# Performance work log

Hardware: AMD Instinct MI355X
Metric: run time of the kernel (lower is better)

The kernel has to match this reference:

```python
import jax, jax.numpy as jnp
import numpy as np

S, N, CM, CZ, H, D = 512, 768, 64, 128, 8, 32
EPS = 1e-5


def _layer_norm(x, w, b):
    mu = jnp.mean(x, axis=-1, keepdims=True)
    xc = x - mu
    var = jnp.mean(xc * xc, axis=-1, keepdims=True)
    return xc * jax.lax.rsqrt(var + EPS) * w + b


def setup_inputs() -> dict:
    key = jax.random.key(0)
    ks = jax.random.split(key, 6)
    scale_m = 1.0 / np.sqrt(CM)
    scale_z = 1.0 / np.sqrt(CZ)
    scale_o = 1.0 / np.sqrt(H * D)
    return {
        "m": jax.random.normal(ks[0], (1, S, N, CM), jnp.float32),
        "z": jax.random.normal(ks[1], (1, N, N, CZ), jnp.float32),
        "norm_m_w": jnp.ones((CM,), jnp.float32),
        "norm_m_b": jnp.zeros((CM,), jnp.float32),
        "norm_z_w": jnp.ones((CZ,), jnp.float32),
        "norm_z_b": jnp.zeros((CZ,), jnp.float32),
        "wm": jax.random.normal(ks[2], (CM, H * D), jnp.float32) * scale_m,
        "wg": jax.random.normal(ks[3], (CM, H * D), jnp.float32) * scale_m,
        "wz": jax.random.normal(ks[4], (CZ, H), jnp.float32) * scale_z,
        "wo": jax.random.normal(ks[5], (H * D, CM), jnp.float32) * scale_o,
    }


def reference(m, z, norm_m_w, norm_m_b, norm_z_w, norm_z_b, wm, wg, wz, wo):
    m0 = m[0]  # [S, N, CM]
    z0 = z[0]  # [N, N, CZ]
    mn = _layer_norm(m0, norm_m_w, norm_m_b)
    zn = _layer_norm(z0, norm_z_w, norm_z_b)
    # b[p,q,h]; original code softmaxes over the LAST axis of b'[h,p,q] (axis q)
    # but contracts as o[s,q] = sum_p w[p,q] v[s,p] (transpose_a matmul),
    # so softmax is over axis q = axis 1 of [p,q,h].
    b = jnp.einsum('pqc,ch->pqh', zn, wz)
    w = jax.nn.softmax(b, axis=1)  # normalized over q for each p (faithful to source)
    v = jnp.einsum('spc,ck->spk', mn, wm).reshape(S, N, H, D)
    g = jax.nn.sigmoid(jnp.einsum('spc,ck->spk', mn, wg)).reshape(S, N, H, D)
    o = jnp.einsum('pqh,sphd->sqhd', w, v) * g  # weighted average then gate
    out = jnp.einsum('sqhd,hdc->sqc', o, wo.reshape(H, D, CM))
    return out[None]  # [1, S, N, CM]
```

## Files before the change

### kernel.cpp

```cpp
#include <hip/hip_runtime.h>
#include <hip/hip_bf16.h>
#include <stdint.h>

#define S_DIM 512
#define N_DIM 768
#define CMd   64
#define CZd   128
#define Hd    8
#define Dd    32
#define HDd   256

typedef float          f32x4  __attribute__((ext_vector_type(4)));
typedef __bf16         bf16x8 __attribute__((ext_vector_type(8)));
typedef unsigned int   u32x4  __attribute__((ext_vector_type(4)));
typedef unsigned int   u32x2  __attribute__((ext_vector_type(2)));
typedef unsigned short u16x8  __attribute__((ext_vector_type(8)));

__device__ __forceinline__ unsigned short f2bf(float f) {
  __bf16 h = (__bf16)f;
  return __builtin_bit_cast(unsigned short, h);
}
__device__ __forceinline__ float bf2f(unsigned short u) {
  unsigned int x = ((unsigned int)u) << 16;
  return __builtin_bit_cast(float, x);
}
__device__ __forceinline__ float sigmoidf_(float x) {
  return 1.f / (1.f + __expf(-x));
}

__global__ __launch_bounds__(256) void k0_prep(const float* __restrict__ wm,
                                               const float* __restrict__ wg,
                                               const float* __restrict__ wo,
                                               unsigned short* __restrict__ WBT,
                                               unsigned short* __restrict__ woT) {
  int t = blockIdx.x * 256 + threadIdx.x;
  if (t < 512 * 64) {
    int j = t >> 6, c = t & 63;
    float v = (j < 256) ? wm[c * 256 + j] : wg[c * 256 + (j - 256)];
    WBT[t] = f2bf(v);
  }
  if (t < 64 * 256) {
    int c = t >> 8, k = t & 255;
    woT[t] = f2bf(wo[k * 64 + c]);
  }
}

__global__ __launch_bounds__(256) void k1_zln_b(const float* __restrict__ z,
                                                const float* __restrict__ nzw,
                                                const float* __restrict__ nzb,
                                                const float* __restrict__ wz,
                                                float* __restrict__ b_e) {
  __shared__ float wzT[8][128];
  int t = threadIdx.x;
  for (int i = t; i < 1024; i += 256) {
    int h = i >> 7, c = i & 127;
    wzT[h][c] = wz[c * 8 + h];
  }
  __syncthreads();

  int lane = t & 63, w = t >> 6;
  int sub = lane & 7;
  int rloc = lane >> 3;
  int p = blockIdx.y;
  int q = blockIdx.x * 32 + w * 8 + rloc;

  const float* zr = z + ((size_t)p * N_DIM + q) * CZd + sub * 16;
  f32x4 v[4];
#pragma unroll
  for (int j = 0; j < 4; j++) v[j] = *(const f32x4*)(zr + 4 * j);

  float s1 = 0.f, s2 = 0.f;
#pragma unroll
  for (int j = 0; j < 4; j++)
#pragma unroll
    for (int e = 0; e < 4; e++) { float x = v[j][e]; s1 += x; s2 += x * x; }
  s1 += __shfl_xor(s1, 1); s2 += __shfl_xor(s2, 1);
  s1 += __shfl_xor(s1, 2); s2 += __shfl_xor(s2, 2);
  s1 += __shfl_xor(s1, 4); s2 += __shfl_xor(s2, 4);
  float mean = s1 * (1.f / 128.f);
  float var  = s2 * (1.f / 128.f) - mean * mean;
  float rstd = rsqrtf(var + 1e-5f);

  const float* wp = nzw + sub * 16;
  const float* bp = nzb + sub * 16;
  float zn[16];
#pragma unroll
  for (int j = 0; j < 4; j++) {
    f32x4 wv = *(const f32x4*)(wp + 4 * j);
    f32x4 bv = *(const f32x4*)(bp + 4 * j);
#pragma unroll
    for (int e = 0; e < 4; e++)
      zn[j * 4 + e] = (v[j][e] - mean) * rstd * wv[e] + bv[e];
  }

  float accb[8];
#pragma unroll
  for (int h = 0; h < 8; h++) {
    const f32x4* wr = (const f32x4*)&wzT[h][sub * 16];
    float a = 0.f;
#pragma unroll
    for (int j = 0; j < 4; j++) {
      f32x4 ww = wr[j];
#pragma unroll
      for (int e = 0; e < 4; e++) a += zn[j * 4 + e] * ww[e];
    }
    accb[h] = a;
  }
#pragma unroll
  for (int mask = 1; mask <= 4; mask <<= 1)
#pragma unroll
    for (int h = 0; h < 8; h++) accb[h] += __shfl_xor(accb[h], mask);

  float outv = accb[0];
#pragma unroll
  for (int h = 1; h < 8; h++) outv = (sub == h) ? accb[h] : outv;
  b_e[((size_t)p * 8 + sub) * 768 + q] = outv;
}

__global__ __launch_bounds__(256) void k1b_softmax(float* __restrict__ b_e,
                                                   float* __restrict__ invs) {
  int row = blockIdx.x;
  int t = threadIdx.x;
  float* base = b_e + (size_t)row * 768;
  float x0 = base[t], x1 = base[t + 256], x2 = base[t + 512];
  __shared__ float red[256];
  red[t] = fmaxf(x0, fmaxf(x1, x2));
  __syncthreads();
  for (int o = 128; o > 0; o >>= 1) {
    if (t < o) red[t] = fmaxf(red[t], red[t + o]);
    __syncthreads();
  }
  float M = red[0];
  __syncthreads();
  float e0 = __expf(x0 - M), e1 = __expf(x1 - M), e2 = __expf(x2 - M);
  base[t] = e0; base[t + 256] = e1; base[t + 512] = e2;
  red[t] = e0 + e1 + e2;
  __syncthreads();
  for (int o = 128; o > 0; o >>= 1) {
    if (t < o) red[t] += red[t + o];
    __syncthreads();
  }
  if (t == 0) invs[row] = 1.0f / red[0];
}

__global__ __launch_bounds__(256) void k1b2_transpose(const float* __restrict__ b_e,
                                                      const float* __restrict__ invs,
                                                      unsigned short* __restrict__ Aw) {
  int t = threadIdx.x;
  int q0 = blockIdx.x * 64, p0 = blockIdx.y * 64, h = blockIdx.z;
  __shared__ unsigned short T[64][65];
  int i = t >> 2, ch = t & 3;
  size_t rowid = (size_t)(p0 + i) * 8 + h;
  const float* src = b_e + rowid * 768 + q0 + ch * 16;
  float inv = invs[rowid];
#pragma unroll
  for (int jj = 0; jj < 16; jj += 4) {
    f32x4 v = *(const f32x4*)(src + jj);
#pragma unroll
    for (int e = 0; e < 4; e++) T[i][ch * 16 + jj + e] = f2bf(v[e] * inv);
  }
  __syncthreads();
  int j = i;
  unsigned short outv[16];
#pragma unroll
  for (int ii = 0; ii < 16; ii++) outv[ii] = T[ch * 16 + ii][j];
  unsigned short* dst = Aw + ((size_t)h * 768 + q0 + j) * 768 + p0 + ch * 16;
  *(u32x4*)(dst)     = *(u32x4*)(outv);
  *(u32x4*)(dst + 8) = *(u32x4*)(outv + 8);
}

__global__ __launch_bounds__(256) void k2_mln_vg(const float* __restrict__ mp,
                                                 const float* __restrict__ nmw,
                                                 const float* __restrict__ nmb,
                                                 const unsigned short* __restrict__ WBT,
                                                 unsigned short* __restrict__ VT,
                                                 unsigned short* __restrict__ G) {
  __shared__ unsigned short WBs[512 * 64];
  __shared__ unsigned short As[64 * 64];
  int t = threadIdx.x;
  int p0 = blockIdx.x * 64, s = blockIdx.y;

#pragma unroll
  for (int it = 0; it < 16; it++) {
    int cid = t + it * 256;
    int row = cid >> 3, ch = cid & 7;
    u32x4 v = *(const u32x4*)(WBT + row * 64 + ch * 8);
    *(u32x4*)(WBs + row * 64 + ((ch * 8) ^ ((row & 7) << 3))) = v;
  }

  {
    int row = t >> 2, qt = t & 3;
    const float* mr = mp + ((size_t)s * N_DIM + p0 + row) * CMd + qt * 16;
    f32x4 v[4];
#pragma unroll
    for (int j = 0; j < 4; j++) v[j] = *(const f32x4*)(mr + 4 * j);
    float s1 = 0.f, s2 = 0.f;
#pragma unroll
    for (int j = 0; j < 4; j++)
#pragma unroll
      for (int e = 0; e < 4; e++) { float x = v[j][e]; s1 += x; s2 += x * x; }
    s1 += __shfl_xor(s1, 1); s2 += __shfl_xor(s2, 1);
    s1 += __shfl_xor(s1, 2); s2 += __shfl_xor(s2, 2);
    float mean = s1 * (1.f / 64.f);
    float var  = s2 * (1.f / 64.f) - mean * mean;
    float rstd = rsqrtf(var + 1e-5f);
    unsigned short o[16];
#pragma unroll
    for (int j = 0; j < 4; j++) {
      f32x4 wv = *(const f32x4*)(nmw + qt * 16 + 4 * j);
      f32x4 bv = *(const f32x4*)(nmb + qt * 16 + 4 * j);
#pragma unroll
      for (int e = 0; e < 4; e++)
        o[j * 4 + e] = f2bf((v[j][e] - mean) * rstd * wv[e] + bv[e]);
    }
    int k0 = qt * 16;
    *(u32x4*)(As + row * 64 + ((k0) ^ ((row & 7) << 3)))     = *(u32x4*)(o);
    *(u32x4*)(As + row * 64 + ((k0 + 8) ^ ((row & 7) << 3))) = *(u32x4*)(o + 8);
  }
  __syncthreads();

  int lane = t & 63, w = t >> 6;
  int n0 = w * 128;
  int lr = lane & 15, lk8 = (lane >> 4) * 8;
  f32x4 zero = {0.f, 0.f, 0.f, 0.f};
  f32x4 acc[4][8];
#pragma unroll
  for (int i = 0; i < 4; i++)
#pragma unroll
    for (int j = 0; j < 8; j++) acc[i][j] = zero;

#pragma unroll
  for (int kk = 0; kk < 2; kk++) {
    bf16x8 bfr[8];
#pragma unroll
    for (int nt = 0; nt < 8; nt++) {
      int r = n0 + nt * 16 + lr;
      bfr[nt] = *(const bf16x8*)(WBs + r * 64 + ((kk * 32 + lk8) ^ ((r & 7) << 3)));
    }
#pragma unroll
    for (int mt = 0; mt < 4; mt++) {
      int ar = mt * 16 + lr;
      bf16x8 a = *(const bf16x8*)(As + ar * 64 + ((kk * 32 + lk8) ^ ((ar & 7) << 3)));
#pragma unroll
      for (int nt = 0; nt < 8; nt++)
        acc[mt][nt] = __builtin_amdgcn_mfma_f32_16x16x32_bf16(a, bfr[nt], acc[mt][nt], 0, 0, 0);
    }
  }

#pragma unroll
  for (int mt = 0; mt < 4; mt++)
#pragma unroll
    for (int nt = 0; nt < 8; nt++) {
      int j = n0 + nt * 16 + lr;
      int ploc = mt * 16 + (lane >> 4) * 4;
      if (j < 256) {
        int h = j >> 5, d = j & 31;
        unsigned short pk[4];
#pragma unroll
        for (int r = 0; r < 4; r++) pk[r] = f2bf(acc[mt][nt][r]);
        *(u32x2*)(VT + ((size_t)h * 16384 + s * 32 + d) * 768 + p0 + ploc) = *(u32x2*)pk;
      } else {
        int jj = j - 256;
#pragma unroll
        for (int r = 0; r < 4; r++)
          G[((size_t)s * 768 + p0 + ploc + r) * 256 + jj] = f2bf(sigmoidf_(acc[mt][nt][r]));
      }
    }
}

__global__ __launch_bounds__(256) void k3_gemm(const unsigned short* __restrict__ Aw,
                                               const unsigned short* __restrict__ VT,
                                               unsigned short* __restrict__ O) {
  __shared__ unsigned short Asl[128 * 64];
  __shared__ unsigned short Bsl[128 * 64];
  int t = threadIdx.x;
  int flat = blockIdx.x;
  int h = blockIdx.y;
  int f2 = (flat & 7) * 96 + (flat >> 3);
  int mt_b = f2 % 6, nt_b = f2 / 6;
  int q0 = mt_b * 128, n0 = nt_b * 128;

  const unsigned short* Ab = Aw + (size_t)h * 768 * 768 + (size_t)q0 * 768;
  const unsigned short* Bb = VT + (size_t)h * 16384 * 768 + (size_t)n0 * 768;

  int lane = t & 63, w = t >> 6;
  int wr = (w >> 1) * 64, wc = (w & 1) * 64;
  int lr = lane & 15, lk8 = (lane >> 4) * 8;
  int ch = t & 7, r0 = t >> 3;

  u32x4 ra[4], rb[4];
#pragma unroll
  for (int it = 0; it < 4; it++) {
    int r = r0 + it * 32;
    ra[it] = *(const u32x4*)(Ab + (size_t)r * 768 + ch * 8);
    rb[it] = *(const u32x4*)(Bb + (size_t)r * 768 + ch * 8);
  }

  f32x4 zero = {0.f, 0.f, 0.f, 0.f};
  f32x4 acc[4][4];
#pragma unroll
  for (int i = 0; i < 4; i++)
#pragma unroll
    for (int j = 0; j < 4; j++) acc[i][j] = zero;

  for (int kt = 0; kt < 12; kt++) {
#pragma unroll
    for (int it = 0; it < 4; it++) {
      int cid = t + it * 256;
      int row = cid >> 3, c = cid & 7;
      int idx = row * 64 + ((c * 8) ^ ((row & 7) << 3));
      *(u32x4*)(Asl + idx) = ra[it];
      *(u32x4*)(Bsl + idx) = rb[it];
    }
    __syncthreads();
    if (kt < 11) {
      int k0 = (kt + 1) * 64;
#pragma unroll
      for (int it = 0; it < 4; it++) {
        int r = r0 + it * 32;
        ra[it] = *(const u32x4*)(Ab + (size_t)r * 768 + k0 + ch * 8);
        rb[it] = *(const u32x4*)(Bb + (size_t)r * 768 + k0 + ch * 8);
      }
    }
#pragma unroll
    for (int kk = 0; kk < 2; kk++) {
      bf16x8 afr[4], bfr[4];
#pragma unroll
      for (int i = 0; i < 4; i++) {
        int arr = wr + i * 16 + lr;
        int brr = wc + i * 16 + lr;
        afr[i] = *(const bf16x8*)(Asl + arr * 64 + ((kk * 32 + lk8) ^ ((arr & 7) << 3)));
        bfr[i] = *(const bf16x8*)(Bsl + brr * 64 + ((kk * 32 + lk8) ^ ((brr & 7) << 3)));
      }
#pragma unroll
      for (int mt = 0; mt < 4; mt++)
#pragma unroll
        for (int nt = 0; nt < 4; nt++)
          acc[mt][nt] = __builtin_amdgcn_mfma_f32_16x16x32_bf16(afr[mt], bfr[nt], acc[mt][nt], 0, 0, 0);
    }
    __syncthreads();
  }

#pragma unroll
  for (int mt = 0; mt < 4; mt++)
#pragma unroll
    for (int nt = 0; nt < 4; nt++) {
      int q = q0 + wr + mt * 16 + (lane >> 4) * 4;
      int n = n0 + wc + nt * 16 + lr;
      int s_ = n >> 5, d = n & 31;
      size_t ob = ((size_t)s_ * 768 + q) * 256 + h * 32 + d;
#pragma unroll
      for (int r = 0; r < 4; r++)
        O[ob + (size_t)r * 256] = f2bf(acc[mt][nt][r]);
    }
}

__global__ __launch_bounds__(256) void k4_out(const unsigned short* __restrict__ O,
                                              const unsigned short* __restrict__ G,
                                              const unsigned short* __restrict__ woT,
                                              float* __restrict__ out) {
  __shared__ unsigned short OGs[64 * 256];
  __shared__ unsigned short WOs[64 * 256];
  int t = threadIdx.x;
  int q0 = blockIdx.x * 64, s = blockIdx.y;

#pragma unroll
  for (int it = 0; it < 8; it++) {
    int cid = t + it * 256;
    int row = cid >> 5, ch = cid & 31;
    u32x4 v = *(const u32x4*)(woT + row * 256 + ch * 8);
    *(u32x4*)(WOs + row * 256 + ((ch * 8) ^ ((row & 7) << 3))) = v;
  }

  int i = t >> 2, c4 = t & 3;
  const unsigned short* Orow = O + ((size_t)s * 768 + q0 + i) * 256 + c4 * 64;
  const unsigned short* Grow = G + ((size_t)s * 768 + q0 + i) * 256 + c4 * 64;
#pragma unroll
  for (int jj = 0; jj < 8; jj++) {
    u16x8 ov = *(const u16x8*)(Orow + jj * 8);
    u16x8 gv = *(const u16x8*)(Grow + jj * 8);
    unsigned short pk[8];
#pragma unroll
    for (int e = 0; e < 8; e++) pk[e] = f2bf(bf2f(ov[e]) * bf2f(gv[e]));
    *(u32x4*)(OGs + i * 256 + ((c4 * 64 + jj * 8) ^ ((i & 7) << 3))) = *(u32x4*)pk;
  }
  __syncthreads();

  int lane = t & 63, w = t >> 6;
  int lr = lane & 15, lk8 = (lane >> 4) * 8;
  f32x4 zero = {0.f, 0.f, 0.f, 0.f};
  f32x4 acc[4];
#pragma unroll
  for (int nt = 0; nt < 4; nt++) acc[nt] = zero;

#pragma unroll
  for (int kk = 0; kk < 8; kk++) {
    int ar = w * 16 + lr;
    bf16x8 a = *(const bf16x8*)(OGs + ar * 256 + ((kk * 32 + lk8) ^ ((ar & 7) << 3)));
#pragma unroll
    for (int nt = 0; nt < 4; nt++) {
      int br = nt * 16 + lr;
      bf16x8 b = *(const bf16x8*)(WOs + br * 256 + ((kk * 32 + lk8) ^ ((br & 7) << 3)));
      acc[nt] = __builtin_amdgcn_mfma_f32_16x16x32_bf16(a, b, acc[nt], 0, 0, 0);
    }
  }

#pragma unroll
  for (int nt = 0; nt < 4; nt++) {
    int q = q0 + w * 16 + (lane >> 4) * 4;
    int c = nt * 16 + lr;
    float* dst = out + ((size_t)s * 768 + q) * 64 + c;
#pragma unroll
    for (int r = 0; r < 4; r++) dst[(size_t)r * 64] = acc[nt][r];
  }
}

extern "C" void kernel_launch(void* const* d_in, const int* in_sizes, int n_in,
                              void* d_out, int out_size, void* d_ws, size_t ws_size,
                              hipStream_t stream) {
  const float* m   = (const float*)d_in[0];
  const float* z   = (const float*)d_in[1];
  const float* nmw = (const float*)d_in[2];
  const float* nmb = (const float*)d_in[3];
  const float* nzw = (const float*)d_in[4];
  const float* nzb = (const float*)d_in[5];
  const float* wm  = (const float*)d_in[6];
  const float* wg  = (const float*)d_in[7];
  const float* wz  = (const float*)d_in[8];
  const float* wo  = (const float*)d_in[9];
  float* out = (float*)d_out;

  char* ws = (char*)d_ws;
  size_t off = 0;
  auto alloc = [&](size_t bytes) -> void* {
    void* p = ws + off;
    off += (bytes + 1023) & ~(size_t)1023;
    return p;
  };
  float*          b_e  = (float*)alloc((size_t)768 * 8 * 768 * 4);
  float*          invs = (float*)alloc((size_t)768 * 8 * 4);
  unsigned short* Awt  = (unsigned short*)alloc((size_t)8 * 768 * 768 * 2);
  unsigned short* WBT  = (unsigned short*)alloc((size_t)512 * 64 * 2);
  unsigned short* woT  = (unsigned short*)alloc((size_t)64 * 256 * 2);
  unsigned short* VT   = (unsigned short*)alloc((size_t)8 * 16384 * 768 * 2);
  unsigned short* G    = (unsigned short*)alloc((size_t)512 * 768 * 256 * 2);
  unsigned short* O    = (unsigned short*)alloc((size_t)512 * 768 * 256 * 2);
  if (ws_size < off) return;

  k0_prep<<<128, 256, 0, stream>>>(wm, wg, wo, WBT, woT);
  k1_zln_b<<<dim3(24, 768), 256, 0, stream>>>(z, nzw, nzb, wz, b_e);
  k1b_softmax<<<6144, 256, 0, stream>>>(b_e, invs);
  k1b2_transpose<<<dim3(12, 12, 8), 256, 0, stream>>>(b_e, invs, Awt);
  k2_mln_vg<<<dim3(12, 512), 256, 0, stream>>>(m, nmw, nmb, WBT, VT, G);
  k3_gemm<<<dim3(768, 8), 256, 0, stream>>>(Awt, VT, O);
  k4_out<<<dim3(12, 512), 256, 0, stream>>>(O, G, woT, out);
}
```

Baseline: 693.5 us.

## Load GEMM tiles directly into LDS with global_load_lds using pre-swizzled layouts

The producer kernels now write Aw and VT in a layout that is already XOR-swizzled within each 64-element block. This lets the main GEMM copy tiles straight from global memory into LDS with 16-byte global_load_lds, with no register staging and no swizzle at LDS-write time. The aim is to save VGPRs and LDS write instructions. In exchange, the old register prefetch of the next k-tile is gone: each iteration waits on vmcnt(0) before computing, so load latency is no longer overlapped with MFMA work, and the layout is now coupled across kernels.

```diff
diff --git a/kernel.cpp b/kernel.cpp
--- a/kernel.cpp
+++ b/kernel.cpp
@@ -26,6 +26,12 @@
 }
 __device__ __forceinline__ float sigmoidf_(float x) {
   return 1.f / (1.f + __expf(-x));
+}
+
+typedef __attribute__((address_space(1))) const void cg_void;
+typedef __attribute__((address_space(3))) void lds_void;
+__device__ __forceinline__ void async16(const unsigned short* g, unsigned short* l) {
+  __builtin_amdgcn_global_load_lds((cg_void*)g, (lds_void*)l, 16, 0, 0);
 }
 
 __global__ __launch_bounds__(256) void k0_prep(const float* __restrict__ wm,
@@ -164,9 +170,10 @@
   unsigned short outv[16];
 #pragma unroll
   for (int ii = 0; ii < 16; ii++) outv[ii] = T[ch * 16 + ii][j];
-  unsigned short* dst = Aw + ((size_t)h * 768 + q0 + j) * 768 + p0 + ch * 16;
-  *(u32x4*)(dst)     = *(u32x4*)(outv);
-  *(u32x4*)(dst + 8) = *(u32x4*)(outv + 8);
+  int rx = (j & 7) << 3;
+  unsigned short* dstrow = Aw + ((size_t)h * 768 + q0 + j) * 768 + p0;
+  *(u32x4*)(dstrow + ((ch * 16) ^ rx))     = *(u32x4*)(outv);
+  *(u32x4*)(dstrow + ((ch * 16 + 8) ^ rx)) = *(u32x4*)(outv + 8);
 }
 
 __global__ __launch_bounds__(256) void k2_mln_vg(const float* __restrict__ mp,
@@ -258,7 +265,8 @@
         unsigned short pk[4];
 #pragma unroll
         for (int r = 0; r < 4; r++) pk[r] = f2bf(acc[mt][nt][r]);
-        *(u32x2*)(VT + ((size_t)h * 16384 + s * 32 + d) * 768 + p0 + ploc) = *(u32x2*)pk;
+        int pswz = ((((ploc >> 3) ^ (lr & 7)) << 3) | (ploc & 7));
+        *(u32x2*)(VT + ((size_t)h * 16384 + s * 32 + d) * 768 + p0 + pswz) = *(u32x2*)pk;
       } else {
         int jj = j - 256;
 #pragma unroll
@@ -285,16 +293,12 @@
 
   int lane = t & 63, w = t >> 6;
   int wr = (w >> 1) * 64, wc = (w & 1) * 64;
-  int lr = lane & 15, lk8 = (lane >> 4) * 8;
-  int ch = t & 7, r0 = t >> 3;
-
-  u32x4 ra[4], rb[4];
-#pragma unroll
-  for (int it = 0; it < 4; it++) {
-    int r = r0 + it * 32;
-    ra[it] = *(const u32x4*)(Ab + (size_t)r * 768 + ch * 8);
-    rb[it] = *(const u32x4*)(Bb + (size_t)r * 768 + ch * 8);
-  }
+  int lr = lane & 15;
+
+  const unsigned short* gA = Ab + (size_t)(w * 32 + (lane >> 3)) * 768 + (lane & 7) * 8;
+  const unsigned short* gB = Bb + (size_t)(w * 32 + (lane >> 3)) * 768 + (lane & 7) * 8;
+  unsigned short* lA = Asl + w * 2048;
+  unsigned short* lB = Bsl + w * 2048;
 
   f32x4 zero = {0.f, 0.f, 0.f, 0.f};
   f32x4 acc[4][4];
@@ -304,33 +308,25 @@
     for (int j = 0; j < 4; j++) acc[i][j] = zero;
 
   for (int kt = 0; kt < 12; kt++) {
-#pragma unroll
-    for (int it = 0; it < 4; it++) {
-      int cid = t + it * 256;
-      int row = cid >> 3, c = cid & 7;
-      int idx = row * 64 + ((c * 8) ^ ((row & 7) << 3));
-      *(u32x4*)(Asl + idx) = ra[it];
-      *(u32x4*)(Bsl + idx) = rb[it];
-    }
+    int ko = kt * 64;
+#pragma unroll
+    for (int i = 0; i < 4; i++) {
+      async16(gA + (size_t)i * 8 * 768 + ko, lA + i * 512);
+      async16(gB + (size_t)i * 8 * 768 + ko, lB + i * 512);
+    }
+    asm volatile("s_waitcnt vmcnt(0)" ::: "memory");
+    __builtin_amdgcn_sched_barrier(0);
     __syncthreads();
-    if (kt < 11) {
-      int k0 = (kt + 1) * 64;
-#pragma unroll
-      for (int it = 0; it < 4; it++) {
-        int r = r0 + it * 32;
-        ra[it] = *(const u32x4*)(Ab + (size_t)r * 768 + k0 + ch * 8);
-        rb[it] = *(const u32x4*)(Bb + (size_t)r * 768 + k0 + ch * 8);
-      }
-    }
 #pragma unroll
     for (int kk = 0; kk < 2; kk++) {
+      int kc = kk * 32 + (lane >> 4) * 8;
       bf16x8 afr[4], bfr[4];
 #pragma unroll
       for (int i = 0; i < 4; i++) {
         int arr = wr + i * 16 + lr;
         int brr = wc + i * 16 + lr;
-        afr[i] = *(const bf16x8*)(Asl + arr * 64 + ((kk * 32 + lk8) ^ ((arr & 7) << 3)));
-        bfr[i] = *(const bf16x8*)(Bsl + brr * 64 + ((kk * 32 + lk8) ^ ((brr & 7) << 3)));
+        afr[i] = *(const bf16x8*)(Asl + arr * 64 + (kc ^ ((arr & 7) << 3)));
+        bfr[i] = *(const bf16x8*)(Bsl + brr * 64 + (kc ^ ((brr & 7) << 3)));
       }
 #pragma unroll
       for (int mt = 0; mt < 4; mt++)
```

After: 694.6 us. No clear change (+0.2%).
